# Kernel tuning notes

Measured on AMD Instinct MI355X. Metric: run time of the kernel, lower is better.

The kernel has to match this reference:

```python
import jax, jax.numpy as jnp
import numpy as np

B, L, D = 4096, 64, 128
NUM_IDS = 1000


def setup_inputs() -> dict:
    key = jax.random.key(0)
    ks = jax.random.split(key, 8)
    src_node_ids = jax.random.randint(ks[0], (B,), 0, NUM_IDS, dtype=jnp.int32)
    dst_node_ids = jax.random.randint(ks[1], (B,), 0, NUM_IDS, dtype=jnp.int32)
    src_nb = jax.random.randint(ks[2], (B, L), 0, NUM_IDS, dtype=jnp.int32)
    dst_nb = jax.random.randint(ks[3], (B, L), 0, NUM_IDS, dtype=jnp.int32)
    # MLP params: Linear(1 -> D), ReLU, Linear(D -> D)
    W1 = jax.random.normal(ks[4], (1, D), dtype=jnp.float32) / jnp.sqrt(1.0)
    b1 = jnp.zeros((D,), dtype=jnp.float32)
    W2 = jax.random.normal(ks[5], (D, D), dtype=jnp.float32) / jnp.sqrt(D)
    b2 = jnp.zeros((D,), dtype=jnp.float32)
    return {
        "src_node_ids": src_node_ids,
        "dst_node_ids": dst_node_ids,
        "src_nodes_neighbor_ids": src_nb,
        "dst_nodes_neighbor_ids": dst_nb,
        "W1": W1, "b1": b1, "W2": W2, "b2": b2,
    }


def _appearances(src_id, dst_id, src_nb, dst_nb):
    # counts of each neighbor within its own list: (B, L)
    c_src = (src_nb[:, :, None] == src_nb[:, None, :]).sum(-1)
    c_dst = (dst_nb[:, :, None] == dst_nb[:, None, :]).sum(-1)
    # cross counts: count of src neighbor in dst list and vice versa
    c_dst_of_src = (src_nb[:, :, None] == dst_nb[:, None, :]).sum(-1)  # (B, L)
    c_src_of_dst = (dst_nb[:, :, None] == src_nb[:, None, :]).sum(-1)  # (B, L)
    # scalar per batch: count of src_id in dst list, dst_id in src list
    cd_srcid = (dst_nb == src_id[:, None]).sum(-1)  # (B,)
    cs_dstid = (src_nb == dst_id[:, None]).sum(-1)  # (B,)
    srcid_in_dst = cd_srcid > 0
    same = src_id == dst_id
    # dict-mutation semantics of count_nodes_appearances:
    # src_mapping[src_id] overwritten with cd_srcid when src_id in dst list
    # dst_mapping[dst_id] overwritten with (post-mutation) src_mapping[dst_id]
    cond2 = (cs_dstid > 0) | (same & srcid_in_dst)
    v2 = jnp.where(same & srcid_in_dst, cd_srcid, cs_dstid)
    # dst_mapping.get(src neighbors): count in dst, with dst_id override
    src_col1 = jnp.where((src_nb == dst_id[:, None]) & cond2[:, None],
                         v2[:, None], c_dst_of_src)
    # src_mapping.get(dst neighbors): count in src, with src_id override
    dst_col0 = jnp.where((dst_nb == src_id[:, None]) & srcid_in_dst[:, None],
                         cd_srcid[:, None], c_src_of_dst)
    src_app = jnp.stack([c_src, src_col1], axis=-1).astype(jnp.float32)  # (B,L,2)
    dst_app = jnp.stack([dst_col0, c_dst], axis=-1).astype(jnp.float32)  # (B,L,2)
    return src_app, dst_app


def _mlp(app, W1, b1, W2, b2):
    # app: (B, L, 2) -> (B, L, 2, D) -> sum over the 2 co-occurrence channels
    h = jax.nn.relu(app[..., None] * W1[0] + b1)      # (B, L, 2, D)
    out = jnp.einsum('blcd,de->blce', h, W2) + b2     # (B, L, 2, D)
    return out.sum(axis=2)                            # (B, L, D)


def reference(src_node_ids, dst_node_ids, src_nodes_neighbor_ids,
              dst_nodes_neighbor_ids, W1, b1, W2, b2):
    src_app, dst_app = _appearances(src_node_ids, dst_node_ids,
                                    src_nodes_neighbor_ids, dst_nodes_neighbor_ids)
    src_feat = _mlp(src_app, W1, b1, W2, b2)
    dst_feat = _mlp(dst_app, W1, b1, W2, b2)
    return src_feat, dst_feat
```

## Files before the change

kernel.cpp:

```cpp
#include <hip/hip_runtime.h>

#define DD   128
#define LLEN 64
#define TMAX 65

__global__ void build_table_kernel(const float* __restrict__ W1,
                                   const float* __restrict__ b1,
                                   const float* __restrict__ W2,
                                   float* __restrict__ tab) {
    const int a = blockIdx.x;
    const int e = threadIdx.x;
    const float fa = (float)a;
    float acc = 0.f;
#pragma unroll 8
    for (int d = 0; d < DD; ++d) {
        float h = fmaf(fa, W1[d], b1[d]);
        h = fmaxf(h, 0.f);
        acc = fmaf(h, W2[d * DD + e], acc);
    }
    tab[a * DD + e] = acc;
}

__global__ __launch_bounds__(256) void nif_main_kernel(
    const int* __restrict__ src_id, const int* __restrict__ dst_id,
    const int* __restrict__ src_nb, const int* __restrict__ dst_nb,
    const float* __restrict__ tab, const float* __restrict__ b2,
    float* __restrict__ out, int B) {
    __shared__ int S[LLEN], Dn[LLEN];
    __shared__ int A0[LLEN], A1[LLEN], C0[LLEN], C1[LLEN];

    const int b = blockIdx.x;
    const int tid = threadIdx.x;

    if (tid < LLEN)          S[tid]         = src_nb[(size_t)b * LLEN + tid];
    else if (tid < 2 * LLEN) Dn[tid - LLEN] = dst_nb[(size_t)b * LLEN + (tid - LLEN)];
    __syncthreads();

    if (tid < LLEN) {
        const int sid = src_id[b];
        const int did = dst_id[b];
        const int vs = S[tid];
        const int vd = Dn[tid];
        int c_src = 0, c_dos = 0, c_dst = 0, c_sod = 0, cd_sid = 0, cs_did = 0;
#pragma unroll
        for (int j = 0; j < LLEN; ++j) {
            const int sj = S[j], dj = Dn[j];
            c_src  += (sj == vs);
            c_dos  += (dj == vs);
            c_dst  += (dj == vd);
            c_sod  += (sj == vd);
            cd_sid += (dj == sid);
            cs_did += (sj == did);
        }
        const bool s_in_d = (cd_sid > 0);
        const bool same   = (sid == did);
        const bool c2     = (cs_did > 0) || (same && s_in_d);
        const int  v2     = (same && s_in_d) ? cd_sid : cs_did;
        A0[tid] = c_src;
        A1[tid] = (vs == did && c2) ? v2 : c_dos;
        C0[tid] = (vd == sid && s_in_d) ? cd_sid : c_sod;
        C1[tid] = c_dst;
    }
    __syncthreads();

    const float4* __restrict__ tab4 = (const float4*)tab;
    float4 b2v = ((const float4*)b2)[tid & 31];
    b2v.x += b2v.x; b2v.y += b2v.y; b2v.z += b2v.z; b2v.w += b2v.w;

    float4* __restrict__ out4 = (float4*)out;
    const size_t src_base = (size_t)b * (LLEN * DD / 4);
    const size_t dst_base = src_base + (size_t)B * (LLEN * DD / 4);
    const int e4 = tid & 31;
    const int l0 = tid >> 5;
#pragma unroll
    for (int k = 0; k < 8; ++k) {
        const int l = l0 + 8 * k;
        const int idx4 = l * 32 + e4;
        const float4 t0 = tab4[A0[l] * 32 + e4];
        const float4 t1 = tab4[A1[l] * 32 + e4];
        float4 v;
        v.x = t0.x + t1.x + b2v.x;
        v.y = t0.y + t1.y + b2v.y;
        v.z = t0.z + t1.z + b2v.z;
        v.w = t0.w + t1.w + b2v.w;
        out4[src_base + idx4] = v;
        const float4 u0 = tab4[C0[l] * 32 + e4];
        const float4 u1 = tab4[C1[l] * 32 + e4];
        float4 w;
        w.x = u0.x + u1.x + b2v.x;
        w.y = u0.y + u1.y + b2v.y;
        w.z = u0.z + u1.z + b2v.z;
        w.w = u0.w + u1.w + b2v.w;
        out4[dst_base + idx4] = w;
    }
}

extern "C" void kernel_launch(void* const* d_in, const int* in_sizes, int n_in,
                              void* d_out, int out_size, void* d_ws, size_t ws_size,
                              hipStream_t stream) {
    const int*   src_id = (const int*)d_in[0];
    const int*   dst_id = (const int*)d_in[1];
    const int*   src_nb = (const int*)d_in[2];
    const int*   dst_nb = (const int*)d_in[3];
    const float* W1     = (const float*)d_in[4];
    const float* b1     = (const float*)d_in[5];
    const float* W2     = (const float*)d_in[6];
    const float* b2     = (const float*)d_in[7];
    float*       out    = (float*)d_out;
    float*       tab    = (float*)d_ws;

    const int B = in_sizes[0];

    build_table_kernel<<<TMAX, DD, 0, stream>>>(W1, b1, W2, tab);
    nif_main_kernel<<<B, 256, 0, stream>>>(src_id, dst_id, src_nb, dst_nb,
                                           tab, b2, out, B);
}
```

Baseline: 289.8 us.

## Process four batch rows per block with one wavefront each and ballot counts

Each 256-thread block now handles four batch rows, one 64-lane wavefront per row, instead of one row per block. Before, only a quarter of the threads did the count phase while the others waited. Now every lane does counting, and the scalar id counts use ballot plus popcount instead of loop accumulation. Each wavefront then writes its own row's outputs, which are 64 float4 lines per half. The risk is that the grid has four times fewer blocks and the code assumes B is divisible by four.

```diff
diff --git a/kernel.cpp b/kernel.cpp
--- a/kernel.cpp
+++ b/kernel.cpp
@@ -3,6 +3,7 @@
 #define DD   128
 #define LLEN 64
 #define TMAX 65
+#define ROWS_PER_BLK 4
 
 __global__ void build_table_kernel(const float* __restrict__ W1,
                                    const float* __restrict__ b1,
@@ -14,8 +15,7 @@
     float acc = 0.f;
 #pragma unroll 8
     for (int d = 0; d < DD; ++d) {
-        float h = fmaf(fa, W1[d], b1[d]);
-        h = fmaxf(h, 0.f);
+        float h = fmaxf(fmaf(fa, W1[d], b1[d]), 0.f);
         acc = fmaf(h, W2[d * DD + e], acc);
     }
     tab[a * DD + e] = acc;
@@ -26,72 +26,75 @@
     const int* __restrict__ src_nb, const int* __restrict__ dst_nb,
     const float* __restrict__ tab, const float* __restrict__ b2,
     float* __restrict__ out, int B) {
-    __shared__ int S[LLEN], Dn[LLEN];
-    __shared__ int A0[LLEN], A1[LLEN], C0[LLEN], C1[LLEN];
+    __shared__ int S[ROWS_PER_BLK][LLEN], Dn[ROWS_PER_BLK][LLEN];
+    __shared__ int A0[ROWS_PER_BLK][LLEN], A1[ROWS_PER_BLK][LLEN];
+    __shared__ int C0[ROWS_PER_BLK][LLEN], C1[ROWS_PER_BLK][LLEN];
 
-    const int b = blockIdx.x;
-    const int tid = threadIdx.x;
+    const int tid  = threadIdx.x;
+    const int w    = tid >> 6;
+    const int lane = tid & 63;
+    const int b    = blockIdx.x * ROWS_PER_BLK + w;
 
-    if (tid < LLEN)          S[tid]         = src_nb[(size_t)b * LLEN + tid];
-    else if (tid < 2 * LLEN) Dn[tid - LLEN] = dst_nb[(size_t)b * LLEN + (tid - LLEN)];
+    S[w][lane]  = src_nb[(size_t)b * LLEN + lane];
+    Dn[w][lane] = dst_nb[(size_t)b * LLEN + lane];
     __syncthreads();
 
-    if (tid < LLEN) {
+    {
         const int sid = src_id[b];
         const int did = dst_id[b];
-        const int vs = S[tid];
-        const int vd = Dn[tid];
-        int c_src = 0, c_dos = 0, c_dst = 0, c_sod = 0, cd_sid = 0, cs_did = 0;
-#pragma unroll
+        const int vs = S[w][lane];
+        const int vd = Dn[w][lane];
+        const int cd_sid = __popcll(__ballot(vd == sid));
+        const int cs_did = __popcll(__ballot(vs == did));
+        int c_src = 0, c_dos = 0, c_dst = 0, c_sod = 0;
+#pragma unroll 8
         for (int j = 0; j < LLEN; ++j) {
-            const int sj = S[j], dj = Dn[j];
-            c_src  += (sj == vs);
-            c_dos  += (dj == vs);
-            c_dst  += (dj == vd);
-            c_sod  += (sj == vd);
-            cd_sid += (dj == sid);
-            cs_did += (sj == did);
+            const int sj = S[w][j], dj = Dn[w][j];
+            c_src += (sj == vs);
+            c_dos += (dj == vs);
+            c_dst += (dj == vd);
+            c_sod += (sj == vd);
         }
         const bool s_in_d = (cd_sid > 0);
         const bool same   = (sid == did);
         const bool c2     = (cs_did > 0) || (same && s_in_d);
         const int  v2     = (same && s_in_d) ? cd_sid : cs_did;
-        A0[tid] = c_src;
-        A1[tid] = (vs == did && c2) ? v2 : c_dos;
-        C0[tid] = (vd == sid && s_in_d) ? cd_sid : c_sod;
-        C1[tid] = c_dst;
+        A0[w][lane] = c_src;
+        A1[w][lane] = (vs == did && c2) ? v2 : c_dos;
+        C0[w][lane] = (vd == sid && s_in_d) ? cd_sid : c_sod;
+        C1[w][lane] = c_dst;
     }
     __syncthreads();
 
     const float4* __restrict__ tab4 = (const float4*)tab;
-    float4 b2v = ((const float4*)b2)[tid & 31];
+    float4 b2v = ((const float4*)b2)[lane & 31];
     b2v.x += b2v.x; b2v.y += b2v.y; b2v.z += b2v.z; b2v.w += b2v.w;
 
     float4* __restrict__ out4 = (float4*)out;
     const size_t src_base = (size_t)b * (LLEN * DD / 4);
     const size_t dst_base = src_base + (size_t)B * (LLEN * DD / 4);
-    const int e4 = tid & 31;
-    const int l0 = tid >> 5;
-#pragma unroll
-    for (int k = 0; k < 8; ++k) {
-        const int l = l0 + 8 * k;
+    const int e4 = lane & 31;
+    const int lh = lane >> 5;
+#pragma unroll 4
+    for (int k = 0; k < 32; ++k) {
+        const int l = 2 * k + lh;
         const int idx4 = l * 32 + e4;
-        const float4 t0 = tab4[A0[l] * 32 + e4];
-        const float4 t1 = tab4[A1[l] * 32 + e4];
+        const float4 t0 = tab4[A0[w][l] * 32 + e4];
+        const float4 t1 = tab4[A1[w][l] * 32 + e4];
         float4 v;
         v.x = t0.x + t1.x + b2v.x;
         v.y = t0.y + t1.y + b2v.y;
         v.z = t0.z + t1.z + b2v.z;
         v.w = t0.w + t1.w + b2v.w;
         out4[src_base + idx4] = v;
-        const float4 u0 = tab4[C0[l] * 32 + e4];
-        const float4 u1 = tab4[C1[l] * 32 + e4];
-        float4 w;
-        w.x = u0.x + u1.x + b2v.x;
-        w.y = u0.y + u1.y + b2v.y;
-        w.z = u0.z + u1.z + b2v.z;
-        w.w = u0.w + u1.w + b2v.w;
-        out4[dst_base + idx4] = w;
+        const float4 u0 = tab4[C0[w][l] * 32 + e4];
+        const float4 u1 = tab4[C1[w][l] * 32 + e4];
+        float4 wv;
+        wv.x = u0.x + u1.x + b2v.x;
+        wv.y = u0.y + u1.y + b2v.y;
+        wv.z = u0.z + u1.z + b2v.z;
+        wv.w = u0.w + u1.w + b2v.w;
+        out4[dst_base + idx4] = wv;
     }
 }
 
@@ -112,6 +115,6 @@
     const int B = in_sizes[0];
 
     build_table_kernel<<<TMAX, DD, 0, stream>>>(W1, b1, W2, tab);
-    nif_main_kernel<<<B, 256, 0, stream>>>(src_id, dst_id, src_nb, dst_nb,
-                                           tab, b2, out, B);
+    nif_main_kernel<<<B / ROWS_PER_BLK, 256, 0, stream>>>(
+        src_id, dst_id, src_nb, dst_nb, tab, b2, out, B);
 }
```

After: 280.7 us. -3.1%, faster.
